# Kernel tuning notes

Measured on AMD Instinct MI355X. Metric: run time of the kernel, lower is better.

The kernel has to match this reference:

```python
import jax, jax.numpy as jnp
import numpy as np

TEMPERATURE = 0.1


def setup_inputs() -> dict:
    key = jax.random.key(0)
    k1, k2 = jax.random.split(key)
    N, T, D = 4096, 4, 256
    v_feat = jax.random.normal(k1, (N, D), dtype=jnp.float32)
    t_feat = jax.random.normal(k2, (N * T, D), dtype=jnp.float32)
    return {"v_feat": v_feat, "t_feat": t_feat}


def reference(v_feat, t_feat):
    N, D = v_feat.shape
    NT = t_feat.shape[0]
    T = NT // N

    # similarity matrix, scaled by temperature: [N, N*T]
    s_flat = (v_feat @ t_feat.T) / TEMPERATURE
    s = s_flat.reshape(N, N, T)

    # nominator: diagonal blocks s[i, i, :] -> logsumexp over T
    # (equivalent to (s * eye[:, :, None]).sum(dim=1))
    diag = jnp.diagonal(s, axis1=0, axis2=1).T  # [N, T]
    nominator = jax.nn.logsumexp(diag, axis=1)  # [N]

    # denominator: concat(s, s^T) along dim 1 -> [N, 2N, T] -> logsumexp over flat
    denom_in = jnp.concatenate([s, jnp.transpose(s, (1, 0, 2))], axis=1).reshape(N, -1)
    denominator = jax.nn.logsumexp(denom_in, axis=1)  # [N]

    mil_nce_loss = jnp.mean(denominator - nominator)

    # --- metrics (no grad), vectorized replacement of the python loop ---
    # rank[i, j] = index (into N*T columns) of the j-th largest score for row i
    rank = jnp.argsort(-s_flat, axis=1)  # [N, N*T], descending
    # column c belongs to video c // T; positive hit where that equals row index i
    hit = (rank // T) == jnp.arange(N)[:, None]  # [N, N*T] bool
    positions = jnp.arange(NT, dtype=jnp.float32)
    avg_rank = jnp.sum(hit.astype(jnp.float32) * positions, axis=1) / T
    recall1 = jnp.sum(hit[:, :1].astype(jnp.float32), axis=1) / T
    recall5 = jnp.sum(hit[:, :5].astype(jnp.float32), axis=1) / T
    recall10 = jnp.sum(hit[:, :10].astype(jnp.float32), axis=1) / T

    return (mil_nce_loss,
            jnp.mean(recall1), jnp.mean(recall5), jnp.mean(recall10),
            jnp.mean(avg_rank))
```

## Files before the change

### kernel.cpp

```cpp
#include <hip/hip_runtime.h>
#include <stdint.h>

#define N_V   4096
#define T_PER 4
#define NT    16384
#define D_K   256
#define SCALE 10.0f
#define LOG2E 1.44269504088896340736f
#define LN2   0.69314718055994530942f

#if defined(__has_builtin)
#if __has_builtin(__builtin_amdgcn_exp2f)
#define EXP2F(x) __builtin_amdgcn_exp2f(x)
#endif
#endif
#ifndef EXP2F
#define EXP2F(x) exp2f(x)
#endif

typedef __bf16 bf16x8 __attribute__((ext_vector_type(8)));
typedef float  f32x4  __attribute__((ext_vector_type(4)));

template<int C>
__device__ __forceinline__ float dppf(float v) {
  return __int_as_float(__builtin_amdgcn_update_dpp(
      0, __float_as_int(v), C, 0xf, 0xf, true));
}
template<int C>
__device__ __forceinline__ uint32_t dppu(uint32_t v) {
  return (uint32_t)__builtin_amdgcn_update_dpp(0, (int)v, C, 0xf, 0xf, true);
}
__device__ __forceinline__ float max16(float v) {
  v = fmaxf(v, dppf<0x121>(v));
  v = fmaxf(v, dppf<0x122>(v));
  v = fmaxf(v, dppf<0x124>(v));
  v = fmaxf(v, dppf<0x128>(v));
  return v;
}
__device__ __forceinline__ float sum16f(float v) {
  v += dppf<0x121>(v); v += dppf<0x122>(v);
  v += dppf<0x124>(v); v += dppf<0x128>(v);
  return v;
}
__device__ __forceinline__ uint32_t sum16u(uint32_t v) {
  v += dppu<0x121>(v); v += dppu<0x122>(v);
  v += dppu<0x124>(v); v += dppu<0x128>(v);
  return v;
}

__device__ __forceinline__ unsigned short f2bf(float f) {
  uint32_t u = __float_as_uint(f);
  u = (u + 0x7fffu + ((u >> 16) & 1u)) >> 16;
  return (unsigned short)u;
}

__global__ void k_prep(const float* __restrict__ v, const float* __restrict__ t,
                       unsigned short* __restrict__ Abf, unsigned short* __restrict__ Bbf,
                       float* __restrict__ thr, float* __restrict__ thmin,
                       float* __restrict__ nom, float* __restrict__ out) {
  const int tid = threadIdx.x, l = tid & 63, w = tid >> 6;
  const int i = blockIdx.x * 4 + w;
  if (blockIdx.x == 0 && tid < 5) out[tid] = 0.0f;
  const float AS = SCALE * LOG2E;

  float4 a = ((const float4*)(v + (size_t)i * D_K))[l];
  ushort4 oa;
  oa.x = f2bf(a.x * AS); oa.y = f2bf(a.y * AS);
  oa.z = f2bf(a.z * AS); oa.w = f2bf(a.w * AS);
  ((ushort4*)(Abf + (size_t)i * D_K))[l] = oa;

  float tv[T_PER];
#pragma unroll
  for (int tt = 0; tt < T_PER; ++tt) {
    float4 b = ((const float4*)(t + (size_t)(i * T_PER + tt) * D_K))[l];
    ushort4 ob;
    ob.x = f2bf(b.x); ob.y = f2bf(b.y); ob.z = f2bf(b.z); ob.w = f2bf(b.w);
    ((ushort4*)(Bbf + (size_t)(i * T_PER + tt) * D_K))[l] = ob;
    float d = a.x * b.x + a.y * b.y + a.z * b.z + a.w * b.w;
#pragma unroll
    for (int s = 1; s < 64; s <<= 1) d += __shfl_xor(d, s);
    tv[tt] = d * SCALE;
  }
  if (l == 0) {
    ((float4*)thr)[i] = make_float4(tv[0] * LOG2E, tv[1] * LOG2E,
                                    tv[2] * LOG2E, tv[3] * LOG2E);
    thmin[i] = fminf(fminf(tv[0], tv[1]), fminf(tv[2], tv[3])) * LOG2E;
    float m = fmaxf(fmaxf(tv[0], tv[1]), fmaxf(tv[2], tv[3]));
    float e = __expf(tv[0] - m) + __expf(tv[1] - m) + __expf(tv[2] - m) + __expf(tv[3] - m);
    nom[i] = m + __logf(e);
  }
}

__device__ __forceinline__ void gld16(const void* g, void* l) {
  __builtin_amdgcn_global_load_lds((const __attribute__((address_space(1))) void*)g,
                                   (__attribute__((address_space(3))) void*)l,
                                   16, 0, 0);
}

__global__ __launch_bounds__(256, 4) void k_gemm(
    const unsigned short* __restrict__ Abf, const unsigned short* __restrict__ Bbf,
    const float* __restrict__ thr, const float* __restrict__ thmin,
    float* __restrict__ pmax, float* __restrict__ psum, uint4* __restrict__ pcnt,
    float* __restrict__ cmax, float* __restrict__ csum) {
  __shared__ __align__(16) unsigned short As[64 * 256];
  __shared__ float4   thrS[64];
  __shared__ float    thminS[64];
  __shared__ float    rowMw[4][64], rowEw[4][64];
  __shared__ uint32_t rowCw[4][64];

  const int ct = blockIdx.x, rt = blockIdx.y;
  const int row0 = rt * 64, col0 = ct * 256;
  const int tid = threadIdx.x;
  const int l = tid & 63, w = tid >> 6;
  const int quad = l >> 4, nl = l & 15;

  if (tid < 64) {
    thrS[tid] = ((const float4*)thr)[row0 + tid];
    thminS[tid] = thmin[row0 + tid];
  }

  const int lr = l >> 3, lc7 = l & 7;
  const int sc = lc7 ^ lr;
#pragma unroll
  for (int it = 0; it < 8; ++it) {
    int g = w * 8 + it;
    int rs = g >> 2, ks = g & 3;
    const unsigned short* ga =
        Abf + (size_t)(row0 + rs * 8 + lr) * D_K + ks * 64 + sc * 8;
    gld16(ga, (char*)As + g * 1024);
  }

  f32x4 acc[4][4];
#pragma unroll
  for (int i = 0; i < 4; ++i)
#pragma unroll
    for (int j = 0; j < 4; ++j) acc[i][j] = {0.f, 0.f, 0.f, 0.f};

  const unsigned short* pB[4];
#pragma unroll
  for (int j = 0; j < 4; ++j)
    pB[j] = Bbf + (size_t)(col0 + w * 64 + j * 16 + nl) * D_K + quad * 8;

  __syncthreads();

  bf16x8 bv[3][4];
#pragma unroll
  for (int j = 0; j < 4; ++j) bv[0][j] = *(const bf16x8*)(pB[j]);
#pragma unroll
  for (int j = 0; j < 4; ++j) bv[1][j] = *(const bf16x8*)(pB[j] + 32);

#pragma unroll
  for (int c = 0; c < 8; ++c) {
    if (c < 6) {
#pragma unroll
      for (int j = 0; j < 4; ++j)
        bv[(c + 2) % 3][j] = *(const bf16x8*)(pB[j] + (c + 2) * 32);
    }
    bf16x8 af[4];
#pragma unroll
    for (int i = 0; i < 4; ++i) {
      int r = i * 16 + nl;
      int rb = r & 7;
      int grp = (r >> 3) * 4 + (c >> 1);
      int cc = ((((c & 1) << 2) | quad) ^ rb);
      af[i] = *(const bf16x8*)((const char*)As + grp * 1024 + (rb * 8 + cc) * 16);
    }
#pragma unroll
    for (int i = 0; i < 4; ++i)
#pragma unroll
      for (int j = 0; j < 4; ++j)
        acc[i][j] = __builtin_amdgcn_mfma_f32_16x16x32_bf16(af[i], bv[c % 3][j],
                                                            acc[i][j], 0, 0, 0);
  }


#pragma unroll
  for (int i = 0; i < 4; ++i) {
#pragma unroll
    for (int r = 0; r < 4; ++r) {
      const int row = i * 16 + quad * 4 + r;
      float s0 = acc[i][0][r], s1 = acc[i][1][r];
      float s2 = acc[i][2][r], s3 = acc[i][3][r];
      float m = fmaxf(fmaxf(s0, s1), fmaxf(s2, s3));
      m = max16(m);
      uint32_t c = 0;
      if (__any(m > thminS[row])) {
        float4 th = thrS[row];
        uint32_t c0 = (uint32_t)(s0 > th.x) + (uint32_t)(s1 > th.x)
                    + (uint32_t)(s2 > th.x) + (uint32_t)(s3 > th.x);
        uint32_t c1 = (uint32_t)(s0 > th.y) + (uint32_t)(s1 > th.y)
                    + (uint32_t)(s2 > th.y) + (uint32_t)(s3 > th.y);
        uint32_t c2 = (uint32_t)(s0 > th.z) + (uint32_t)(s1 > th.z)
                    + (uint32_t)(s2 > th.z) + (uint32_t)(s3 > th.z);
        uint32_t c3 = (uint32_t)(s0 > th.w) + (uint32_t)(s1 > th.w)
                    + (uint32_t)(s2 > th.w) + (uint32_t)(s3 > th.w);
        c = c0 + (c1 << 8) + (c2 << 16) + (c3 << 24);
        c = sum16u(c);
      }
      float e = EXP2F(s0 - m) + EXP2F(s1 - m) + EXP2F(s2 - m) + EXP2F(s3 - m);
      e = sum16f(e);
      if (nl == 0) {
        rowMw[w][row] = m; rowEw[w][row] = e; rowCw[w][row] = c;
      }
    }
  }

#pragma unroll
  for (int j = 0; j < 4; ++j) {
    float m = -3.0e38f;
#pragma unroll
    for (int i = 0; i < 4; ++i)
#pragma unroll
      for (int r = 0; r < 4; ++r) m = fmaxf(m, acc[i][j][r]);
    m = fmaxf(m, __shfl_xor(m, 16));
    m = fmaxf(m, __shfl_xor(m, 32));
    float e = 0.f;
#pragma unroll
    for (int i = 0; i < 4; ++i)
#pragma unroll
      for (int r = 0; r < 4; ++r) e += EXP2F(acc[i][j][r] - m);
    e += __shfl_xor(e, 16);
    e += __shfl_xor(e, 32);
    if (quad == 0) {
      int colg = col0 + w * 64 + j * 16 + nl;
      size_t gi = (size_t)rt * NT + colg;
      cmax[gi] = m; csum[gi] = e;
    }
  }
  __syncthreads();

  if (tid < 64) {
    float M0 = rowMw[0][tid], M1 = rowMw[1][tid], M2 = rowMw[2][tid], M3 = rowMw[3][tid];
    float Mx = fmaxf(fmaxf(M0, M1), fmaxf(M2, M3));
    float Sx = rowEw[0][tid] * EXP2F(M0 - Mx) + rowEw[1][tid] * EXP2F(M1 - Mx)
             + rowEw[2][tid] * EXP2F(M2 - Mx) + rowEw[3][tid] * EXP2F(M3 - Mx);
    uint32_t c0 = 0, c1 = 0, c2 = 0, c3 = 0;
#pragma unroll
    for (int ww = 0; ww < 4; ++ww) {
      uint32_t cc = rowCw[ww][tid];
      c0 += cc & 0xffu; c1 += (cc >> 8) & 0xffu;
      c2 += (cc >> 16) & 0xffu; c3 += cc >> 24;
    }
    size_t gi = (size_t)ct * N_V + row0 + tid;
    pmax[gi] = Mx; psum[gi] = Sx; pcnt[gi] = make_uint4(c0, c1, c2, c3);
  }
}

__global__ void k_red(const float* __restrict__ pmax, const float* __restrict__ psum,
                      const uint4* __restrict__ pcnt,
                      const float* __restrict__ cmax, const float* __restrict__ csum,
                      float* __restrict__ rowm, float* __restrict__ rows_,
                      uint4* __restrict__ rcnt,
                      float* __restrict__ colm, float* __restrict__ cols) {
  __shared__ float Lm[4][64], Ls[4][64];
  __shared__ uint4 Lc[4][64];
  __shared__ float Cm[2][128], Cs[2][128];
  const int bid = blockIdx.x, tid = threadIdx.x;
  if (bid < 64) {
    int l = tid & 63, w = tid >> 6;
    int row = bid * 64 + l;
    float mv[16];
#pragma unroll
    for (int k = 0; k < 16; ++k)
      mv[k] = pmax[(size_t)(w * 16 + k) * N_V + row];
    float tm[8];
#pragma unroll
    for (int k = 0; k < 8; ++k) tm[k] = fmaxf(mv[k], mv[k + 8]);
#pragma unroll
    for (int k = 0; k < 4; ++k) tm[k] = fmaxf(tm[k], tm[k + 4]);
    float M = fmaxf(fmaxf(tm[0], tm[1]), fmaxf(tm[2], tm[3]));
    float S = 0.f;
    uint32_t c0 = 0, c1 = 0, c2 = 0, c3 = 0;
#pragma unroll
    for (int k = 0; k < 16; ++k) {
      size_t idx = (size_t)(w * 16 + k) * N_V + row;
      S += psum[idx] * EXP2F(mv[k] - M);
      uint4 cc = pcnt[idx];
      c0 += cc.x; c1 += cc.y; c2 += cc.z; c3 += cc.w;
    }
    Lm[w][l] = M; Ls[w][l] = S; Lc[w][l] = make_uint4(c0, c1, c2, c3);
    __syncthreads();
    if (tid < 64) {
      float M0 = Lm[0][tid], M1 = Lm[1][tid], M2 = Lm[2][tid], M3 = Lm[3][tid];
      float Mx = fmaxf(fmaxf(M0, M1), fmaxf(M2, M3));
      float Sx = Ls[0][tid] * EXP2F(M0 - Mx) + Ls[1][tid] * EXP2F(M1 - Mx)
               + Ls[2][tid] * EXP2F(M2 - Mx) + Ls[3][tid] * EXP2F(M3 - Mx);
      uint4 C = Lc[0][tid];
#pragma unroll
      for (int ww = 1; ww < 4; ++ww) {
        uint4 cc = Lc[ww][tid];
        C.x += cc.x; C.y += cc.y; C.z += cc.z; C.w += cc.w;
      }
      int r = bid * 64 + tid;
      rowm[r] = Mx; rows_[r] = Sx; rcnt[r] = C;
    }
  } else {
    int cb = bid - 64;
    int c = tid & 127, h = tid >> 7;
    int col = cb * 128 + c;
    float mv[32];
#pragma unroll
    for (int k = 0; k < 32; ++k)
      mv[k] = cmax[(size_t)(h * 32 + k) * NT + col];
    float tm[16];
#pragma unroll
    for (int k = 0; k < 16; ++k) tm[k] = fmaxf(mv[k], mv[k + 16]);
#pragma unroll
    for (int k = 0; k < 8; ++k) tm[k] = fmaxf(tm[k], tm[k + 8]);
#pragma unroll
    for (int k = 0; k < 4; ++k) tm[k] = fmaxf(tm[k], tm[k + 4]);
    float M = fmaxf(fmaxf(tm[0], tm[1]), fmaxf(tm[2], tm[3]));
    float S = 0.f;
#pragma unroll
    for (int k = 0; k < 32; ++k)
      S += csum[(size_t)(h * 32 + k) * NT + col] * EXP2F(mv[k] - M);
    Cm[h][c] = M; Cs[h][c] = S;
    __syncthreads();
    if (tid < 128) {
      float M0 = Cm[0][tid], S0 = Cs[0][tid];
      float M1 = Cm[1][tid], S1 = Cs[1][tid];
      float Mx = fmaxf(M0, M1);
      float Sx = S0 * EXP2F(M0 - Mx) + S1 * EXP2F(M1 - Mx);
      int cg = cb * 128 + tid;
      colm[cg] = Mx; cols[cg] = Sx;
    }
  }
}

__global__ void k_final(const float* __restrict__ rowm, const float* __restrict__ rows_,
                        const uint4* __restrict__ rcnt, const float* __restrict__ nom,
                        const float* __restrict__ colm, const float* __restrict__ cols,
                        float* __restrict__ out) {
  int row = blockIdx.x * 256 + threadIdx.x;
  float M = rowm[row], S = rows_[row];
  float cm0 = colm[row * 4 + 0], cm1 = colm[row * 4 + 1];
  float cm2 = colm[row * 4 + 2], cm3 = colm[row * 4 + 3];
  float cs0 = cols[row * 4 + 0], cs1 = cols[row * 4 + 1];
  float cs2 = cols[row * 4 + 2], cs3 = cols[row * 4 + 3];
  float Mp = fmaxf(M, fmaxf(fmaxf(cm0, cm1), fmaxf(cm2, cm3)));
  float tot = S * EXP2F(M - Mp)
            + cs0 * EXP2F(cm0 - Mp) + cs1 * EXP2F(cm1 - Mp)
            + cs2 * EXP2F(cm2 - Mp) + cs3 * EXP2F(cm3 - Mp);
  float ll = LN2 * (Mp + __log2f(tot)) - nom[row];
  uint4 c = rcnt[row];
  float ar  = (float)(c.x + c.y + c.z + c.w) * 0.25f;
  float r1  = (float)((c.x < 1u) + (c.y < 1u) + (c.z < 1u) + (c.w < 1u)) * 0.25f;
  float r5  = (float)((c.x < 5u) + (c.y < 5u) + (c.z < 5u) + (c.w < 5u)) * 0.25f;
  float r10 = (float)((c.x < 10u) + (c.y < 10u) + (c.z < 10u) + (c.w < 10u)) * 0.25f;
  float vals[5] = {ll, r1, r5, r10, ar};
  int l = threadIdx.x & 63;
#pragma unroll
  for (int k = 0; k < 5; ++k) {
    float v = vals[k];
#pragma unroll
    for (int d = 1; d < 64; d <<= 1) v += __shfl_xor(v, d);
    if (l == 0) atomicAdd(&out[k], v * (1.0f / N_V));
  }
}

extern "C" void kernel_launch(void* const* d_in, const int* in_sizes, int n_in,
                              void* d_out, int out_size, void* d_ws, size_t ws_size,
                              hipStream_t stream) {
  const float* v = (const float*)d_in[0];
  const float* t = (const float*)d_in[1];
  char* p = (char*)d_ws;
  unsigned short* Abf = (unsigned short*)p; p += (size_t)N_V * D_K * 2;
  unsigned short* Bbf = (unsigned short*)p; p += (size_t)NT * D_K * 2;
  float* thr  = (float*)p;    p += (size_t)N_V * 4 * 4;
  float* thmn = (float*)p;    p += (size_t)N_V * 4;
  float* nom  = (float*)p;    p += (size_t)N_V * 4;
  float* pmax = (float*)p;    p += (size_t)64 * N_V * 4;
  float* psum = (float*)p;    p += (size_t)64 * N_V * 4;
  uint4* pcnt = (uint4*)p;    p += (size_t)64 * N_V * 16;
  float* cmaxp = (float*)p;   p += (size_t)64 * NT * 4;
  float* csump = (float*)p;   p += (size_t)64 * NT * 4;
  float* rowm = (float*)p;    p += (size_t)N_V * 4;
  float* rows_ = (float*)p;   p += (size_t)N_V * 4;
  uint4* rcnt = (uint4*)p;    p += (size_t)N_V * 16;
  float* colm = (float*)p;    p += (size_t)NT * 4;
  float* cols = (float*)p;    p += (size_t)NT * 4;

  k_prep<<<N_V / 4, 256, 0, stream>>>(v, t, Abf, Bbf, thr, thmn, nom, (float*)d_out);
  dim3 g(NT / 256, N_V / 64);
  k_gemm<<<g, 256, 0, stream>>>(Abf, Bbf, thr, thmn, pmax, psum, pcnt, cmaxp, csump);
  k_red<<<64 + NT / 128, 256, 0, stream>>>(pmax, psum, pcnt, cmaxp, csump,
                                           rowm, rows_, rcnt, colm, cols);
  k_final<<<N_V / 256, 256, 0, stream>>>(rowm, rows_, rcnt, nom, colm, cols, (float*)d_out);
}
```

Before: 157.6 us.

## Fold final reduction into k_red via last-block flag and streamline GEMM epilogue

Removes the separate k_final launch by having the last k_red block, detected with an atomic counter and threadfence, compute the per-row loss and recall metrics and accumulate them into the output. In the GEMM epilogue, the column logsumexp now runs first, using tree reductions and DPP row broadcasts instead of shfl_xor. The per-row threshold counting becomes unconditional, which drops the thmin early-out along with its buffer and loads. This saves one kernel launch and some shuffle latency, but adds a serial tail in one block and always performs the comparison work.

New measurement: 171.9 us. +9.0%, slower.

```diff
diff --git a/kernel.cpp b/kernel.cpp
--- a/kernel.cpp
+++ b/kernel.cpp
@@ -56,11 +56,12 @@
 
 __global__ void k_prep(const float* __restrict__ v, const float* __restrict__ t,
                        unsigned short* __restrict__ Abf, unsigned short* __restrict__ Bbf,
-                       float* __restrict__ thr, float* __restrict__ thmin,
-                       float* __restrict__ nom, float* __restrict__ out) {
+                       float* __restrict__ thr, float* __restrict__ nom,
+                       float* __restrict__ out, uint32_t* __restrict__ flag) {
   const int tid = threadIdx.x, l = tid & 63, w = tid >> 6;
   const int i = blockIdx.x * 4 + w;
   if (blockIdx.x == 0 && tid < 5) out[tid] = 0.0f;
+  if (blockIdx.x == 0 && tid == 5) *flag = 0;
   const float AS = SCALE * LOG2E;
 
   float4 a = ((const float4*)(v + (size_t)i * D_K))[l];
@@ -84,7 +85,6 @@
   if (l == 0) {
     ((float4*)thr)[i] = make_float4(tv[0] * LOG2E, tv[1] * LOG2E,
                                     tv[2] * LOG2E, tv[3] * LOG2E);
-    thmin[i] = fminf(fminf(tv[0], tv[1]), fminf(tv[2], tv[3])) * LOG2E;
     float m = fmaxf(fmaxf(tv[0], tv[1]), fmaxf(tv[2], tv[3]));
     float e = __expf(tv[0] - m) + __expf(tv[1] - m) + __expf(tv[2] - m) + __expf(tv[3] - m);
     nom[i] = m + __logf(e);
@@ -99,12 +99,11 @@
 
 __global__ __launch_bounds__(256, 4) void k_gemm(
     const unsigned short* __restrict__ Abf, const unsigned short* __restrict__ Bbf,
-    const float* __restrict__ thr, const float* __restrict__ thmin,
+    const float* __restrict__ thr,
     float* __restrict__ pmax, float* __restrict__ psum, uint4* __restrict__ pcnt,
     float* __restrict__ cmax, float* __restrict__ csum) {
   __shared__ __align__(16) unsigned short As[64 * 256];
   __shared__ float4   thrS[64];
-  __shared__ float    thminS[64];
   __shared__ float    rowMw[4][64], rowEw[4][64];
   __shared__ uint32_t rowCw[4][64];
 
@@ -114,10 +113,7 @@
   const int l = tid & 63, w = tid >> 6;
   const int quad = l >> 4, nl = l & 15;
 
-  if (tid < 64) {
-    thrS[tid] = ((const float4*)thr)[row0 + tid];
-    thminS[tid] = thmin[row0 + tid];
-  }
+  if (tid < 64) thrS[tid] = ((const float4*)thr)[row0 + tid];
 
   const int lr = l >> 3, lc7 = l & 7;
   const int sc = lc7 ^ lr;
@@ -175,56 +171,65 @@
 
 
 #pragma unroll
+  for (int j = 0; j < 4; ++j) {
+    float x[16];
+#pragma unroll
+    for (int i = 0; i < 4; ++i)
+#pragma unroll
+      for (int r = 0; r < 4; ++r) x[i * 4 + r] = acc[i][j][r];
+    float t8[8];
+#pragma unroll
+    for (int k = 0; k < 8; ++k) t8[k] = fmaxf(x[k], x[k + 8]);
+    float t4[4];
+#pragma unroll
+    for (int k = 0; k < 4; ++k) t4[k] = fmaxf(t8[k], t8[k + 4]);
+    float m = fmaxf(fmaxf(t4[0], t4[1]), fmaxf(t4[2], t4[3]));
+    m = fmaxf(m, dppf<0x142>(m));
+    m = fmaxf(m, dppf<0x143>(m));
+    float ex[16];
+#pragma unroll
+    for (int k = 0; k < 16; ++k) ex[k] = EXP2F(x[k] - m);
+    float s8[8];
+#pragma unroll
+    for (int k = 0; k < 8; ++k) s8[k] = ex[k] + ex[k + 8];
+    float s4[4];
+#pragma unroll
+    for (int k = 0; k < 4; ++k) s4[k] = s8[k] + s8[k + 4];
+    float e = (s4[0] + s4[1]) + (s4[2] + s4[3]);
+    e += dppf<0x142>(e);
+    e += dppf<0x143>(e);
+    if (quad == 3) {
+      int colg = col0 + w * 64 + j * 16 + nl;
+      size_t gi = (size_t)rt * NT + colg;
+      cmax[gi] = m; csum[gi] = e;
+    }
+  }
+
+#pragma unroll
   for (int i = 0; i < 4; ++i) {
 #pragma unroll
     for (int r = 0; r < 4; ++r) {
       const int row = i * 16 + quad * 4 + r;
+      float4 th = thrS[row];
       float s0 = acc[i][0][r], s1 = acc[i][1][r];
       float s2 = acc[i][2][r], s3 = acc[i][3][r];
+      uint32_t c0 = (uint32_t)(s0 > th.x) + (uint32_t)(s1 > th.x)
+                  + (uint32_t)(s2 > th.x) + (uint32_t)(s3 > th.x);
+      uint32_t c1 = (uint32_t)(s0 > th.y) + (uint32_t)(s1 > th.y)
+                  + (uint32_t)(s2 > th.y) + (uint32_t)(s3 > th.y);
+      uint32_t c2 = (uint32_t)(s0 > th.z) + (uint32_t)(s1 > th.z)
+                  + (uint32_t)(s2 > th.z) + (uint32_t)(s3 > th.z);
+      uint32_t c3 = (uint32_t)(s0 > th.w) + (uint32_t)(s1 > th.w)
+                  + (uint32_t)(s2 > th.w) + (uint32_t)(s3 > th.w);
+      uint32_t c = c0 + (c1 << 8) + (c2 << 16) + (c3 << 24);
+      c = sum16u(c);
       float m = fmaxf(fmaxf(s0, s1), fmaxf(s2, s3));
       m = max16(m);
-      uint32_t c = 0;
-      if (__any(m > thminS[row])) {
-        float4 th = thrS[row];
-        uint32_t c0 = (uint32_t)(s0 > th.x) + (uint32_t)(s1 > th.x)
-                    + (uint32_t)(s2 > th.x) + (uint32_t)(s3 > th.x);
-        uint32_t c1 = (uint32_t)(s0 > th.y) + (uint32_t)(s1 > th.y)
-                    + (uint32_t)(s2 > th.y) + (uint32_t)(s3 > th.y);
-        uint32_t c2 = (uint32_t)(s0 > th.z) + (uint32_t)(s1 > th.z)
-                    + (uint32_t)(s2 > th.z) + (uint32_t)(s3 > th.z);
-        uint32_t c3 = (uint32_t)(s0 > th.w) + (uint32_t)(s1 > th.w)
-                    + (uint32_t)(s2 > th.w) + (uint32_t)(s3 > th.w);
-        c = c0 + (c1 << 8) + (c2 << 16) + (c3 << 24);
-        c = sum16u(c);
-      }
-      float e = EXP2F(s0 - m) + EXP2F(s1 - m) + EXP2F(s2 - m) + EXP2F(s3 - m);
+      float e = (EXP2F(s0 - m) + EXP2F(s1 - m)) + (EXP2F(s2 - m) + EXP2F(s3 - m));
       e = sum16f(e);
       if (nl == 0) {
         rowMw[w][row] = m; rowEw[w][row] = e; rowCw[w][row] = c;
       }
-    }
-  }
-
-#pragma unroll
-  for (int j = 0; j < 4; ++j) {
-    float m = -3.0e38f;
-#pragma unroll
-    for (int i = 0; i < 4; ++i)
-#pragma unroll
-      for (int r = 0; r < 4; ++r) m = fmaxf(m, acc[i][j][r]);
-    m = fmaxf(m, __shfl_xor(m, 16));
-    m = fmaxf(m, __shfl_xor(m, 32));
-    float e = 0.f;
-#pragma unroll
-    for (int i = 0; i < 4; ++i)
-#pragma unroll
-      for (int r = 0; r < 4; ++r) e += EXP2F(acc[i][j][r] - m);
-    e += __shfl_xor(e, 16);
-    e += __shfl_xor(e, 32);
-    if (quad == 0) {
-      int colg = col0 + w * 64 + j * 16 + nl;
-      size_t gi = (size_t)rt * NT + colg;
-      cmax[gi] = m; csum[gi] = e;
     }
   }
   __syncthreads();
@@ -251,10 +256,13 @@
                       const float* __restrict__ cmax, const float* __restrict__ csum,
                       float* __restrict__ rowm, float* __restrict__ rows_,
                       uint4* __restrict__ rcnt,
-                      float* __restrict__ colm, float* __restrict__ cols) {
+                      float* __restrict__ colm, float* __restrict__ cols,
+                      const float* __restrict__ nom, float* __restrict__ out,
+                      uint32_t* __restrict__ flag) {
   __shared__ float Lm[4][64], Ls[4][64];
   __shared__ uint4 Lc[4][64];
   __shared__ float Cm[2][128], Cs[2][128];
+  __shared__ uint32_t isLast;
   const int bid = blockIdx.x, tid = threadIdx.x;
   if (bid < 64) {
     int l = tid & 63, w = tid >> 6;
@@ -325,36 +333,45 @@
       colm[cg] = Mx; cols[cg] = Sx;
     }
   }
-}
-
-__global__ void k_final(const float* __restrict__ rowm, const float* __restrict__ rows_,
-                        const uint4* __restrict__ rcnt, const float* __restrict__ nom,
-                        const float* __restrict__ colm, const float* __restrict__ cols,
-                        float* __restrict__ out) {
-  int row = blockIdx.x * 256 + threadIdx.x;
-  float M = rowm[row], S = rows_[row];
-  float cm0 = colm[row * 4 + 0], cm1 = colm[row * 4 + 1];
-  float cm2 = colm[row * 4 + 2], cm3 = colm[row * 4 + 3];
-  float cs0 = cols[row * 4 + 0], cs1 = cols[row * 4 + 1];
-  float cs2 = cols[row * 4 + 2], cs3 = cols[row * 4 + 3];
-  float Mp = fmaxf(M, fmaxf(fmaxf(cm0, cm1), fmaxf(cm2, cm3)));
-  float tot = S * EXP2F(M - Mp)
-            + cs0 * EXP2F(cm0 - Mp) + cs1 * EXP2F(cm1 - Mp)
-            + cs2 * EXP2F(cm2 - Mp) + cs3 * EXP2F(cm3 - Mp);
-  float ll = LN2 * (Mp + __log2f(tot)) - nom[row];
-  uint4 c = rcnt[row];
-  float ar  = (float)(c.x + c.y + c.z + c.w) * 0.25f;
-  float r1  = (float)((c.x < 1u) + (c.y < 1u) + (c.z < 1u) + (c.w < 1u)) * 0.25f;
-  float r5  = (float)((c.x < 5u) + (c.y < 5u) + (c.z < 5u) + (c.w < 5u)) * 0.25f;
-  float r10 = (float)((c.x < 10u) + (c.y < 10u) + (c.z < 10u) + (c.w < 10u)) * 0.25f;
-  float vals[5] = {ll, r1, r5, r10, ar};
-  int l = threadIdx.x & 63;
-#pragma unroll
-  for (int k = 0; k < 5; ++k) {
-    float v = vals[k];
-#pragma unroll
-    for (int d = 1; d < 64; d <<= 1) v += __shfl_xor(v, d);
-    if (l == 0) atomicAdd(&out[k], v * (1.0f / N_V));
+
+  __threadfence();
+  __syncthreads();
+  if (tid == 0) {
+    uint32_t old = atomicAdd(flag, 1u);
+    isLast = (old == 191u);
+  }
+  __syncthreads();
+  if (isLast) {
+    __threadfence();
+    float acc5[5] = {0.f, 0.f, 0.f, 0.f, 0.f};
+#pragma unroll
+    for (int it = 0; it < 16; ++it) {
+      int row = it * 256 + tid;
+      float M = rowm[row], S = rows_[row];
+      float cm0 = colm[row * 4 + 0], cm1 = colm[row * 4 + 1];
+      float cm2 = colm[row * 4 + 2], cm3 = colm[row * 4 + 3];
+      float cs0 = cols[row * 4 + 0], cs1 = cols[row * 4 + 1];
+      float cs2 = cols[row * 4 + 2], cs3 = cols[row * 4 + 3];
+      float Mp = fmaxf(M, fmaxf(fmaxf(cm0, cm1), fmaxf(cm2, cm3)));
+      float tot = S * EXP2F(M - Mp)
+                + cs0 * EXP2F(cm0 - Mp) + cs1 * EXP2F(cm1 - Mp)
+                + cs2 * EXP2F(cm2 - Mp) + cs3 * EXP2F(cm3 - Mp);
+      float ll = LN2 * (Mp + __log2f(tot)) - nom[row];
+      uint4 cc = rcnt[row];
+      acc5[0] += ll;
+      acc5[1] += (float)((cc.x < 1u) + (cc.y < 1u) + (cc.z < 1u) + (cc.w < 1u)) * 0.25f;
+      acc5[2] += (float)((cc.x < 5u) + (cc.y < 5u) + (cc.z < 5u) + (cc.w < 5u)) * 0.25f;
+      acc5[3] += (float)((cc.x < 10u) + (cc.y < 10u) + (cc.z < 10u) + (cc.w < 10u)) * 0.25f;
+      acc5[4] += (float)(cc.x + cc.y + cc.z + cc.w) * 0.25f;
+    }
+    int l = tid & 63;
+#pragma unroll
+    for (int k = 0; k < 5; ++k) {
+      float v = acc5[k];
+#pragma unroll
+      for (int d = 1; d < 64; d <<= 1) v += __shfl_xor(v, d);
+      if (l == 0) atomicAdd(&out[k], v * (1.0f / N_V));
+    }
   }
 }
 
@@ -367,7 +384,6 @@
   unsigned short* Abf = (unsigned short*)p; p += (size_t)N_V * D_K * 2;
   unsigned short* Bbf = (unsigned short*)p; p += (size_t)NT * D_K * 2;
   float* thr  = (float*)p;    p += (size_t)N_V * 4 * 4;
-  float* thmn = (float*)p;    p += (size_t)N_V * 4;
   float* nom  = (float*)p;    p += (size_t)N_V * 4;
   float* pmax = (float*)p;    p += (size_t)64 * N_V * 4;
   float* psum = (float*)p;    p += (size_t)64 * N_V * 4;
@@ -379,11 +395,12 @@
   uint4* rcnt = (uint4*)p;    p += (size_t)N_V * 16;
   float* colm = (float*)p;    p += (size_t)NT * 4;
   float* cols = (float*)p;    p += (size_t)NT * 4;
-
-  k_prep<<<N_V / 4, 256, 0, stream>>>(v, t, Abf, Bbf, thr, thmn, nom, (float*)d_out);
+  uint32_t* flag = (uint32_t*)p; p += 256;
+
+  k_prep<<<N_V / 4, 256, 0, stream>>>(v, t, Abf, Bbf, thr, nom, (float*)d_out, flag);
   dim3 g(NT / 256, N_V / 64);
-  k_gemm<<<g, 256, 0, stream>>>(Abf, Bbf, thr, thmn, pmax, psum, pcnt, cmaxp, csump);
+  k_gemm<<<g, 256, 0, stream>>>(Abf, Bbf, thr, pmax, psum, pcnt, cmaxp, csump);
   k_red<<<64 + NT / 128, 256, 0, stream>>>(pmax, psum, pcnt, cmaxp, csump,
-                                           rowm, rows_, rcnt, colm, cols);
-  k_final<<<N_V / 256, 256, 0, stream>>>(rowm, rows_, rcnt, nom, colm, cols, (float*)d_out);
-}
+                                           rowm, rows_, rcnt, colm, cols,
+                                           nom, (float*)d_out, flag);
+}
```

## Fuse row/column reductions with final loss kernel and drop threshold early-out

Applied to the files above, without the earlier changes.

Merges the separate reduction kernel and final kernel into one k_redfin launch, where each of 64 blocks reduces its 64 rows and the matching 256 columns, then computes the loss and metric contributions directly. This removes one launch and the intermediate rowm/colm round trip through global memory. The GEMM epilogue also drops the per-row min-threshold wave-vote early-out and always computes the threshold counts, which removes a branch and the thmin buffer but adds compare and DPP work on every row. The fused kernel runs only 64 blocks, so the column reduction has less parallelism than the previous 192-block launch.

Result: no change. 156.5 us (-0.7%).

```diff
diff --git a/kernel.cpp b/kernel.cpp
--- a/kernel.cpp
+++ b/kernel.cpp
@@ -56,8 +56,8 @@
 
 __global__ void k_prep(const float* __restrict__ v, const float* __restrict__ t,
                        unsigned short* __restrict__ Abf, unsigned short* __restrict__ Bbf,
-                       float* __restrict__ thr, float* __restrict__ thmin,
-                       float* __restrict__ nom, float* __restrict__ out) {
+                       float* __restrict__ thr, float* __restrict__ nom,
+                       float* __restrict__ out) {
   const int tid = threadIdx.x, l = tid & 63, w = tid >> 6;
   const int i = blockIdx.x * 4 + w;
   if (blockIdx.x == 0 && tid < 5) out[tid] = 0.0f;
@@ -84,7 +84,6 @@
   if (l == 0) {
     ((float4*)thr)[i] = make_float4(tv[0] * LOG2E, tv[1] * LOG2E,
                                     tv[2] * LOG2E, tv[3] * LOG2E);
-    thmin[i] = fminf(fminf(tv[0], tv[1]), fminf(tv[2], tv[3])) * LOG2E;
     float m = fmaxf(fmaxf(tv[0], tv[1]), fmaxf(tv[2], tv[3]));
     float e = __expf(tv[0] - m) + __expf(tv[1] - m) + __expf(tv[2] - m) + __expf(tv[3] - m);
     nom[i] = m + __logf(e);
@@ -99,12 +98,11 @@
 
 __global__ __launch_bounds__(256, 4) void k_gemm(
     const unsigned short* __restrict__ Abf, const unsigned short* __restrict__ Bbf,
-    const float* __restrict__ thr, const float* __restrict__ thmin,
+    const float* __restrict__ thr,
     float* __restrict__ pmax, float* __restrict__ psum, uint4* __restrict__ pcnt,
     float* __restrict__ cmax, float* __restrict__ csum) {
   __shared__ __align__(16) unsigned short As[64 * 256];
   __shared__ float4   thrS[64];
-  __shared__ float    thminS[64];
   __shared__ float    rowMw[4][64], rowEw[4][64];
   __shared__ uint32_t rowCw[4][64];
 
@@ -114,10 +112,7 @@
   const int l = tid & 63, w = tid >> 6;
   const int quad = l >> 4, nl = l & 15;
 
-  if (tid < 64) {
-    thrS[tid] = ((const float4*)thr)[row0 + tid];
-    thminS[tid] = thmin[row0 + tid];
-  }
+  if (tid < 64) thrS[tid] = ((const float4*)thr)[row0 + tid];
 
   const int lr = l >> 3, lc7 = l & 7;
   const int sc = lc7 ^ lr;
@@ -179,25 +174,22 @@
 #pragma unroll
     for (int r = 0; r < 4; ++r) {
       const int row = i * 16 + quad * 4 + r;
+      float4 th = thrS[row];
       float s0 = acc[i][0][r], s1 = acc[i][1][r];
       float s2 = acc[i][2][r], s3 = acc[i][3][r];
+      uint32_t c0 = (uint32_t)(s0 > th.x) + (uint32_t)(s1 > th.x)
+                  + (uint32_t)(s2 > th.x) + (uint32_t)(s3 > th.x);
+      uint32_t c1 = (uint32_t)(s0 > th.y) + (uint32_t)(s1 > th.y)
+                  + (uint32_t)(s2 > th.y) + (uint32_t)(s3 > th.y);
+      uint32_t c2 = (uint32_t)(s0 > th.z) + (uint32_t)(s1 > th.z)
+                  + (uint32_t)(s2 > th.z) + (uint32_t)(s3 > th.z);
+      uint32_t c3 = (uint32_t)(s0 > th.w) + (uint32_t)(s1 > th.w)
+                  + (uint32_t)(s2 > th.w) + (uint32_t)(s3 > th.w);
+      uint32_t c = c0 + (c1 << 8) + (c2 << 16) + (c3 << 24);
+      c = sum16u(c);
       float m = fmaxf(fmaxf(s0, s1), fmaxf(s2, s3));
       m = max16(m);
-      uint32_t c = 0;
-      if (__any(m > thminS[row])) {
-        float4 th = thrS[row];
-        uint32_t c0 = (uint32_t)(s0 > th.x) + (uint32_t)(s1 > th.x)
-                    + (uint32_t)(s2 > th.x) + (uint32_t)(s3 > th.x);
-        uint32_t c1 = (uint32_t)(s0 > th.y) + (uint32_t)(s1 > th.y)
-                    + (uint32_t)(s2 > th.y) + (uint32_t)(s3 > th.y);
-        uint32_t c2 = (uint32_t)(s0 > th.z) + (uint32_t)(s1 > th.z)
-                    + (uint32_t)(s2 > th.z) + (uint32_t)(s3 > th.z);
-        uint32_t c3 = (uint32_t)(s0 > th.w) + (uint32_t)(s1 > th.w)
-                    + (uint32_t)(s2 > th.w) + (uint32_t)(s3 > th.w);
-        c = c0 + (c1 << 8) + (c2 << 16) + (c3 << 24);
-        c = sum16u(c);
-      }
-      float e = EXP2F(s0 - m) + EXP2F(s1 - m) + EXP2F(s2 - m) + EXP2F(s3 - m);
+      float e = (EXP2F(s0 - m) + EXP2F(s1 - m)) + (EXP2F(s2 - m) + EXP2F(s3 - m));
       e = sum16f(e);
       if (nl == 0) {
         rowMw[w][row] = m; rowEw[w][row] = e; rowCw[w][row] = c;
@@ -246,19 +238,21 @@
   }
 }
 
-__global__ void k_red(const float* __restrict__ pmax, const float* __restrict__ psum,
-                      const uint4* __restrict__ pcnt,
-                      const float* __restrict__ cmax, const float* __restrict__ csum,
-                      float* __restrict__ rowm, float* __restrict__ rows_,
-                      uint4* __restrict__ rcnt,
-                      float* __restrict__ colm, float* __restrict__ cols) {
+__global__ void k_redfin(const float* __restrict__ pmax, const float* __restrict__ psum,
+                         const uint4* __restrict__ pcnt,
+                         const float* __restrict__ cmax, const float* __restrict__ csum,
+                         const float* __restrict__ nom, float* __restrict__ out) {
   __shared__ float Lm[4][64], Ls[4][64];
   __shared__ uint4 Lc[4][64];
-  __shared__ float Cm[2][128], Cs[2][128];
-  const int bid = blockIdx.x, tid = threadIdx.x;
-  if (bid < 64) {
-    int l = tid & 63, w = tid >> 6;
-    int row = bid * 64 + l;
+  __shared__ float CmH[2][256], CsH[2][256];
+  __shared__ float rowM[64], rowS[64];
+  __shared__ uint4 rowC[64];
+  __shared__ float colM[256], colS[256];
+  const int b = blockIdx.x, tid = threadIdx.x;
+  const int l = tid & 63, w = tid >> 6;
+
+  {
+    int row = b * 64 + l;
     float mv[16];
 #pragma unroll
     for (int k = 0; k < 16; ++k)
@@ -279,82 +273,82 @@
       c0 += cc.x; c1 += cc.y; c2 += cc.z; c3 += cc.w;
     }
     Lm[w][l] = M; Ls[w][l] = S; Lc[w][l] = make_uint4(c0, c1, c2, c3);
-    __syncthreads();
-    if (tid < 64) {
-      float M0 = Lm[0][tid], M1 = Lm[1][tid], M2 = Lm[2][tid], M3 = Lm[3][tid];
-      float Mx = fmaxf(fmaxf(M0, M1), fmaxf(M2, M3));
-      float Sx = Ls[0][tid] * EXP2F(M0 - Mx) + Ls[1][tid] * EXP2F(M1 - Mx)
-               + Ls[2][tid] * EXP2F(M2 - Mx) + Ls[3][tid] * EXP2F(M3 - Mx);
-      uint4 C = Lc[0][tid];
-#pragma unroll
-      for (int ww = 1; ww < 4; ++ww) {
-        uint4 cc = Lc[ww][tid];
-        C.x += cc.x; C.y += cc.y; C.z += cc.z; C.w += cc.w;
-      }
-      int r = bid * 64 + tid;
-      rowm[r] = Mx; rows_[r] = Sx; rcnt[r] = C;
-    }
-  } else {
-    int cb = bid - 64;
-    int c = tid & 127, h = tid >> 7;
-    int col = cb * 128 + c;
-    float mv[32];
-#pragma unroll
-    for (int k = 0; k < 32; ++k)
-      mv[k] = cmax[(size_t)(h * 32 + k) * NT + col];
-    float tm[16];
-#pragma unroll
-    for (int k = 0; k < 16; ++k) tm[k] = fmaxf(mv[k], mv[k + 16]);
-#pragma unroll
-    for (int k = 0; k < 8; ++k) tm[k] = fmaxf(tm[k], tm[k + 8]);
-#pragma unroll
-    for (int k = 0; k < 4; ++k) tm[k] = fmaxf(tm[k], tm[k + 4]);
-    float M = fmaxf(fmaxf(tm[0], tm[1]), fmaxf(tm[2], tm[3]));
-    float S = 0.f;
-#pragma unroll
-    for (int k = 0; k < 32; ++k)
-      S += csum[(size_t)(h * 32 + k) * NT + col] * EXP2F(mv[k] - M);
-    Cm[h][c] = M; Cs[h][c] = S;
-    __syncthreads();
-    if (tid < 128) {
-      float M0 = Cm[0][tid], S0 = Cs[0][tid];
-      float M1 = Cm[1][tid], S1 = Cs[1][tid];
-      float Mx = fmaxf(M0, M1);
-      float Sx = S0 * EXP2F(M0 - Mx) + S1 * EXP2F(M1 - Mx);
-      int cg = cb * 128 + tid;
-      colm[cg] = Mx; cols[cg] = Sx;
-    }
-  }
-}
-
-__global__ void k_final(const float* __restrict__ rowm, const float* __restrict__ rows_,
-                        const uint4* __restrict__ rcnt, const float* __restrict__ nom,
-                        const float* __restrict__ colm, const float* __restrict__ cols,
-                        float* __restrict__ out) {
-  int row = blockIdx.x * 256 + threadIdx.x;
-  float M = rowm[row], S = rows_[row];
-  float cm0 = colm[row * 4 + 0], cm1 = colm[row * 4 + 1];
-  float cm2 = colm[row * 4 + 2], cm3 = colm[row * 4 + 3];
-  float cs0 = cols[row * 4 + 0], cs1 = cols[row * 4 + 1];
-  float cs2 = cols[row * 4 + 2], cs3 = cols[row * 4 + 3];
-  float Mp = fmaxf(M, fmaxf(fmaxf(cm0, cm1), fmaxf(cm2, cm3)));
-  float tot = S * EXP2F(M - Mp)
-            + cs0 * EXP2F(cm0 - Mp) + cs1 * EXP2F(cm1 - Mp)
-            + cs2 * EXP2F(cm2 - Mp) + cs3 * EXP2F(cm3 - Mp);
-  float ll = LN2 * (Mp + __log2f(tot)) - nom[row];
-  uint4 c = rcnt[row];
-  float ar  = (float)(c.x + c.y + c.z + c.w) * 0.25f;
-  float r1  = (float)((c.x < 1u) + (c.y < 1u) + (c.z < 1u) + (c.w < 1u)) * 0.25f;
-  float r5  = (float)((c.x < 5u) + (c.y < 5u) + (c.z < 5u) + (c.w < 5u)) * 0.25f;
-  float r10 = (float)((c.x < 10u) + (c.y < 10u) + (c.z < 10u) + (c.w < 10u)) * 0.25f;
-  float vals[5] = {ll, r1, r5, r10, ar};
-  int l = threadIdx.x & 63;
-#pragma unroll
-  for (int k = 0; k < 5; ++k) {
-    float v = vals[k];
-#pragma unroll
-    for (int d = 1; d < 64; d <<= 1) v += __shfl_xor(v, d);
-    if (l == 0) atomicAdd(&out[k], v * (1.0f / N_V));
+  }
+
+  {
+    int cc = tid & 127, h = tid >> 7;
+#pragma unroll
+    for (int half = 0; half < 2; ++half) {
+      int colL = half * 128 + cc;
+      int col = b * 256 + colL;
+      float mv[32];
+#pragma unroll
+      for (int k = 0; k < 32; ++k)
+        mv[k] = cmax[(size_t)(h * 32 + k) * NT + col];
+      float tm[16];
+#pragma unroll
+      for (int k = 0; k < 16; ++k) tm[k] = fmaxf(mv[k], mv[k + 16]);
+#pragma unroll
+      for (int k = 0; k < 8; ++k) tm[k] = fmaxf(tm[k], tm[k + 8]);
+#pragma unroll
+      for (int k = 0; k < 4; ++k) tm[k] = fmaxf(tm[k], tm[k + 4]);
+      float M = fmaxf(fmaxf(tm[0], tm[1]), fmaxf(tm[2], tm[3]));
+      float S = 0.f;
+#pragma unroll
+      for (int k = 0; k < 32; ++k)
+        S += csum[(size_t)(h * 32 + k) * NT + col] * EXP2F(mv[k] - M);
+      CmH[h][colL] = M; CsH[h][colL] = S;
+    }
+  }
+  __syncthreads();
+
+  if (tid < 64) {
+    float M0 = Lm[0][tid], M1 = Lm[1][tid], M2 = Lm[2][tid], M3 = Lm[3][tid];
+    float Mx = fmaxf(fmaxf(M0, M1), fmaxf(M2, M3));
+    float Sx = Ls[0][tid] * EXP2F(M0 - Mx) + Ls[1][tid] * EXP2F(M1 - Mx)
+             + Ls[2][tid] * EXP2F(M2 - Mx) + Ls[3][tid] * EXP2F(M3 - Mx);
+    uint4 C = Lc[0][tid];
+#pragma unroll
+    for (int ww = 1; ww < 4; ++ww) {
+      uint4 cc = Lc[ww][tid];
+      C.x += cc.x; C.y += cc.y; C.z += cc.z; C.w += cc.w;
+    }
+    rowM[tid] = Mx; rowS[tid] = Sx; rowC[tid] = C;
+  }
+  {
+    float M0 = CmH[0][tid], S0 = CsH[0][tid];
+    float M1 = CmH[1][tid], S1 = CsH[1][tid];
+    float Mx = fmaxf(M0, M1);
+    float Sx = S0 * EXP2F(M0 - Mx) + S1 * EXP2F(M1 - Mx);
+    colM[tid] = Mx; colS[tid] = Sx;
+  }
+  __syncthreads();
+
+  if (tid < 64) {
+    int row = b * 64 + tid;
+    float M = rowM[tid], S = rowS[tid];
+    float cm0 = colM[tid * 4 + 0], cm1 = colM[tid * 4 + 1];
+    float cm2 = colM[tid * 4 + 2], cm3 = colM[tid * 4 + 3];
+    float cs0 = colS[tid * 4 + 0], cs1 = colS[tid * 4 + 1];
+    float cs2 = colS[tid * 4 + 2], cs3 = colS[tid * 4 + 3];
+    float Mp = fmaxf(M, fmaxf(fmaxf(cm0, cm1), fmaxf(cm2, cm3)));
+    float tot = S * EXP2F(M - Mp)
+              + cs0 * EXP2F(cm0 - Mp) + cs1 * EXP2F(cm1 - Mp)
+              + cs2 * EXP2F(cm2 - Mp) + cs3 * EXP2F(cm3 - Mp);
+    float ll = LN2 * (Mp + __log2f(tot)) - nom[row];
+    uint4 c = rowC[tid];
+    float ar  = (float)(c.x + c.y + c.z + c.w) * 0.25f;
+    float r1  = (float)((c.x < 1u) + (c.y < 1u) + (c.z < 1u) + (c.w < 1u)) * 0.25f;
+    float r5  = (float)((c.x < 5u) + (c.y < 5u) + (c.z < 5u) + (c.w < 5u)) * 0.25f;
+    float r10 = (float)((c.x < 10u) + (c.y < 10u) + (c.z < 10u) + (c.w < 10u)) * 0.25f;
+    float vals[5] = {ll, r1, r5, r10, ar};
+#pragma unroll
+    for (int k = 0; k < 5; ++k) {
+      float v = vals[k];
+#pragma unroll
+      for (int d = 1; d < 64; d <<= 1) v += __shfl_xor(v, d);
+      if (tid == 0) atomicAdd(&out[k], v * (1.0f / N_V));
+    }
   }
 }
 
@@ -367,23 +361,15 @@
   unsigned short* Abf = (unsigned short*)p; p += (size_t)N_V * D_K * 2;
   unsigned short* Bbf = (unsigned short*)p; p += (size_t)NT * D_K * 2;
   float* thr  = (float*)p;    p += (size_t)N_V * 4 * 4;
-  float* thmn = (float*)p;    p += (size_t)N_V * 4;
   float* nom  = (float*)p;    p += (size_t)N_V * 4;
   float* pmax = (float*)p;    p += (size_t)64 * N_V * 4;
   float* psum = (float*)p;    p += (size_t)64 * N_V * 4;
   uint4* pcnt = (uint4*)p;    p += (size_t)64 * N_V * 16;
   float* cmaxp = (float*)p;   p += (size_t)64 * NT * 4;
   float* csump = (float*)p;   p += (size_t)64 * NT * 4;
-  float* rowm = (float*)p;    p += (size_t)N_V * 4;
-  float* rows_ = (float*)p;   p += (size_t)N_V * 4;
-  uint4* rcnt = (uint4*)p;    p += (size_t)N_V * 16;
-  float* colm = (float*)p;    p += (size_t)NT * 4;
-  float* cols = (float*)p;    p += (size_t)NT * 4;
-
-  k_prep<<<N_V / 4, 256, 0, stream>>>(v, t, Abf, Bbf, thr, thmn, nom, (float*)d_out);
+
+  k_prep<<<N_V / 4, 256, 0, stream>>>(v, t, Abf, Bbf, thr, nom, (float*)d_out);
   dim3 g(NT / 256, N_V / 64);
-  k_gemm<<<g, 256, 0, stream>>>(Abf, Bbf, thr, thmn, pmax, psum, pcnt, cmaxp, csump);
-  k_red<<<64 + NT / 128, 256, 0, stream>>>(pmax, psum, pcnt, cmaxp, csump,
-                                           rowm, rows_, rcnt, colm, cols);
-  k_final<<<N_V / 256, 256, 0, stream>>>(rowm, rows_, rcnt, nom, colm, cols, (float*)d_out);
-}
+  k_gemm<<<g, 256, 0, stream>>>(Abf, Bbf, thr, pmax, psum, pcnt, cmaxp, csump);
+  k_redfin<<<64, 256, 0, stream>>>(pmax, psum, pcnt, cmaxp, csump, nom, (float*)d_out);
+}
```
